# Kernel optimization log

Measured on AMD Instinct MI355X. Metric: run time of the kernel, lower is better.

## Reference

```python
import jax, jax.numpy as jnp
import numpy as np

EPS = 1e-5

def adder2d(x, w, stride=1, padding=1):
    # x: [B,C,H,W], w: [O,C,K,K]. AdderNet: out = -sum_{c,kh,kw} |x_patch - w|
    B, C, H, W = x.shape
    O, _, K, _ = w.shape
    xp = jnp.pad(x, ((0, 0), (0, 0), (padding, padding), (padding, padding)))
    Ho = (H + 2 * padding - K) // stride + 1
    Wo = (W + 2 * padding - K) // stride + 1
    out = jnp.zeros((B, O, Ho, Wo), x.dtype)
    for kh in range(K):  # fixed small loop over kernel taps (K*K = 9)
        for kw in range(K):
            xs = xp[:, :, kh:kh + stride * Ho:stride, kw:kw + stride * Wo:stride]  # [B,C,Ho,Wo]
            # broadcasted L1 distance over channel dim: [B,O,C,Ho,Wo] -> sum over C
            out = out - jnp.abs(xs[:, None, :, :, :] - w[None, :, :, kh, kw, None, None]).sum(axis=2)
    return out

def batchnorm(x, gamma, beta, mean, var):
    inv = gamma / jnp.sqrt(var + EPS)
    return x * inv[None, :, None, None] + (beta - mean * inv)[None, :, None, None]

def setup_inputs() -> dict:
    key = jax.random.key(0)
    ks = jax.random.split(key, 8)
    C = 64
    x = jax.random.normal(ks[0], (32, C, 32, 32), dtype=jnp.float32)
    w1 = jax.random.normal(ks[1], (C, C, 3, 3), dtype=jnp.float32) * 0.1
    w2 = jax.random.normal(ks[2], (C, C, 3, 3), dtype=jnp.float32) * 0.1
    bn1_gamma = jax.random.normal(ks[3], (C,), dtype=jnp.float32) * 0.1 + 1.0
    bn1_beta = jax.random.normal(ks[4], (C,), dtype=jnp.float32) * 0.1
    bn1_mean = jax.random.normal(ks[5], (C,), dtype=jnp.float32) * 0.1
    bn1_var = jax.random.uniform(ks[6], (C,), dtype=jnp.float32, minval=0.5, maxval=1.5)
    bn2_gamma = jnp.ones((C,), jnp.float32)
    bn2_beta = jnp.zeros((C,), jnp.float32)
    bn2_mean = jnp.zeros((C,), jnp.float32)
    bn2_var = jax.random.uniform(ks[7], (C,), dtype=jnp.float32, minval=0.5, maxval=1.5)
    return {"x": x, "w1": w1, "w2": w2,
            "bn1_gamma": bn1_gamma, "bn1_beta": bn1_beta, "bn1_mean": bn1_mean, "bn1_var": bn1_var,
            "bn2_gamma": bn2_gamma, "bn2_beta": bn2_beta, "bn2_mean": bn2_mean, "bn2_var": bn2_var}

def reference(x, w1, w2, bn1_gamma, bn1_beta, bn1_mean, bn1_var,
              bn2_gamma, bn2_beta, bn2_mean, bn2_var):
    out = adder2d(jax.nn.relu(batchnorm(x, bn1_gamma, bn1_beta, bn1_mean, bn1_var)), w1, stride=1, padding=1)
    # dropout_rate = 0.0 -> identity
    out = adder2d(jax.nn.relu(batchnorm(out, bn2_gamma, bn2_beta, bn2_mean, bn2_var)), w2, stride=1, padding=1)
    return out + x  # identity shortcut (stride=1, in_planes==planes)
```

## Files before the change

### kernel.cpp

```cpp
#include <hip/hip_runtime.h>
#include <stdint.h>

#define EPS 1e-5f

constexpr int B = 32, C = 64, O = 64, H = 32, W = 32;
constexpr int HP = 34, WP = 34;
constexpr int APLANE = HP * WP;
constexpr int CP = C / 2;
constexpr int AIMG2 = CP * APLANE;
constexpr int ASZ2  = B * AIMG2;
constexpr int WREP2 = (O / 4) * CP * 4 * 9;

constexpr float SCALE = 4096.0f;
constexpr float INV_SCALE = 1.0f / 4096.0f;
constexpr uint32_t ZP16 = 2048u;
constexpr uint32_t ZPAIR = ZP16 | (ZP16 << 16);

__device__ __forceinline__ uint32_t quant_act(float v) {
    return (uint32_t)(v * SCALE + 0.5f) + ZP16;
}
__device__ __forceinline__ uint32_t quant_w(float v) {
    return (uint32_t)(__float2int_rn(v * SCALE) + (int)ZP16);
}

#define SAD16(accv, av, wv) \
    asm("v_sad_u16 %0, %1, %2, %3" : "=v"(accv) : "v"(av), "s"(wv), "0"(accv))

__device__ __forceinline__ bool zero_prop(
    const float* g2, const float* be2, const float* m2, const float* v2)
{
    const int o = threadIdx.x & 63;
    const float inv  = g2[o] / sqrtf(v2[o] + EPS);
    const float bias = be2[o] - m2[o] * inv;
    const bool ok = (inv >= 0.f) && (bias < 0.5f / SCALE);
    return __ballot(ok) == ~0ull;
}

__global__ __launch_bounds__(256) void fused_kernel(
    const float* __restrict__ x,
    const float* __restrict__ w1, const float* __restrict__ w2,
    const float* __restrict__ g1, const float* __restrict__ be1,
    const float* __restrict__ m1, const float* __restrict__ v1,
    const float* __restrict__ g2, const float* __restrict__ be2,
    const float* __restrict__ m2, const float* __restrict__ v2,
    float* __restrict__ out,
    uint32_t* __restrict__ a2p,
    uint32_t* __restrict__ w1r, uint32_t* __restrict__ w2r,
    uint32_t* __restrict__ wsum2, uint32_t* __restrict__ flags,
    float* __restrict__ bn1c, float* __restrict__ bn2c)
{
    if (zero_prop(g2, be2, m2, v2)) {
        const int bo  = blockIdx.x;
        const int o   = bo & 63;
        const int t   = threadIdx.x;
        uint32_t s = 0;
        for (int k = t; k < C * 9; k += 256) {
            const uint32_t q = quant_w(w2[(size_t)o * C * 9 + k]);
            s += (q > ZP16) ? (q - ZP16) : (ZP16 - q);
        }
#pragma unroll
        for (int off = 32; off >= 1; off >>= 1) s += __shfl_down(s, off);
        __shared__ uint32_t red[4];
        if ((t & 63) == 0) red[t >> 6] = s;
        __syncthreads();
        const float wsv = (float)(red[0] + red[1] + red[2] + red[3]) * INV_SCALE;
        const size_t p = (size_t)bo * 256 + t;
        float4 v = ((const float4*)x)[p];
        v.x -= wsv; v.y -= wsv; v.z -= wsv; v.w -= wsv;
        ((float4*)out)[p] = v;
        return;
    }

    const int tid = blockIdx.x * 256 + threadIdx.x;
    const int nth = gridDim.x * 256;

    if (tid < O * 64) {
        const int o  = tid >> 6;
        const int ln = tid & 63;
        uint32_t s = 0;
        for (int k = ln; k < C * 9; k += 64) {
            const uint32_t q = quant_w(w2[(size_t)o * C * 9 + k]);
            s += (q > ZP16) ? (q - ZP16) : (ZP16 - q);
        }
        for (int off = 32; off >= 1; off >>= 1) s += __shfl_down(s, off);
        if (ln == 0) wsum2[o] = s;
    }

    for (int idx = tid; idx < WREP2; idx += nth) {
        const int k  = idx % 9;
        const int t2 = idx / 9;
        const int oi = t2 % 4;
        const int t3 = t2 / 4;
        const int cp = t3 % CP;
        const int og = t3 / CP;
        const int o  = og * 4 + oi;
        const uint32_t lo1 = quant_w(w1[((size_t)o * C + 2 * cp) * 9 + k]);
        const uint32_t hi1 = quant_w(w1[((size_t)o * C + 2 * cp + 1) * 9 + k]);
        const uint32_t lo2 = quant_w(w2[((size_t)o * C + 2 * cp) * 9 + k]);
        const uint32_t hi2 = quant_w(w2[((size_t)o * C + 2 * cp + 1) * 9 + k]);
        w1r[idx] = lo1 | (hi1 << 16);
        w2r[idx] = lo2 | (hi2 << 16);
    }
    if (tid < C) {
        const float i1 = g1[tid] / sqrtf(v1[tid] + EPS);
        bn1c[2 * tid]     = i1;
        bn1c[2 * tid + 1] = be1[tid] - m1[tid] * i1;
        const float i2 = g2[tid] / sqrtf(v2[tid] + EPS);
        bn2c[2 * tid]     = i2;
        bn2c[2 * tid + 1] = be2[tid] - m2[tid] * i2;
    }
    for (int idx = tid; idx < B * H; idx += nth) flags[idx] = 0;

    for (int idx = tid; idx < B * CP * 2 * WP; idx += nth) {
        const int col  = idx % WP;
        const int t2   = idx / WP;
        const int rsel = t2 % 2;
        const int bcp  = t2 / 2;
        a2p[(size_t)bcp * APLANE + (rsel ? HP - 1 : 0) * WP + col] = ZPAIR;
    }
    for (int idx = tid; idx < B * CP * 2 * H; idx += nth) {
        const int rr   = idx % H;
        const int t2   = idx / H;
        const int csel = t2 % 2;
        const int bcp  = t2 / 2;
        a2p[(size_t)bcp * APLANE + (rr + 1) * WP + (csel ? WP - 1 : 0)] = ZPAIR;
    }
}

__global__ __launch_bounds__(1024, 4) void adder1_kernel(
    const float* __restrict__ x, const uint32_t* __restrict__ wr,
    uint32_t* __restrict__ out, const float* __restrict__ bn1c,
    const float* __restrict__ bn2c, uint32_t* __restrict__ flags,
    const float* __restrict__ g2, const float* __restrict__ be2,
    const float* __restrict__ m2, const float* __restrict__ v2)
{
    if (zero_prop(g2, be2, m2, v2)) return;

    const int tid  = threadIdx.x;
    const int lane = tid & 63;
    const int w    = lane & 31;
    const int sub  = lane >> 5;
    const int og      = __builtin_amdgcn_readfirstlane(tid >> 6);
    const int rowbase = blockIdx.x * 4;
    const int b       = blockIdx.y;

    __shared__ uint32_t As[CP][6][WP];
    constexpr int LDSN = CP * 6 * WP;
    const float2* bc1 = (const float2*)bn1c;
#pragma unroll
    for (int i = 0; i < 7; ++i) {
        const int idx = tid + i * 1024;
        if (idx < LDSN) {
            const int col = idx % WP;
            const int seg = idx / WP;
            const int r   = seg % 6;
            const int cp  = seg / 6;
            const int prow = rowbase + r;
            uint32_t q0 = ZP16, q1 = ZP16;
            if (prow >= 1 && prow <= H && col >= 1 && col <= W) {
                const float* xb = x + (((size_t)b * C + 2 * cp) * H + (prow - 1)) * W
                                    + (col - 1);
                const float2 c0 = bc1[2 * cp];
                const float2 c1 = bc1[2 * cp + 1];
                q0 = quant_act(fmaxf(xb[0]     * c0.x + c0.y, 0.f));
                q1 = quant_act(fmaxf(xb[H * W] * c1.x + c1.y, 0.f));
            }
            As[cp][r][col] = q0 | (q1 << 16);
        }
    }
    __syncthreads();

    const uint32_t* wb = wr + (size_t)og * (CP * 36);
    uint32_t acc[4][2] = {};
#pragma unroll
    for (int cp = 0; cp < CP; ++cp) {
        uint32_t wg[36];
#pragma unroll
        for (int k = 0; k < 36; ++k) wg[k] = wb[cp * 36 + k];
#pragma unroll
        for (int kh = 0; kh < 3; ++kh)
#pragma unroll
        for (int kw = 0; kw < 3; ++kw)
#pragma unroll
        for (int oi = 0; oi < 4; ++oi)
#pragma unroll
        for (int r = 0; r < 2; ++r)
            SAD16(acc[oi][r], As[cp][sub * 2 + r + kh][w + kw],
                  wg[oi * 9 + kh * 3 + kw]);
    }

    const int row0 = rowbase + sub * 2;
    const float2* bc2 = (const float2*)bn2c;
    uint32_t qp[2][2];
#pragma unroll
    for (int p = 0; p < 2; ++p) {
        const int o0 = og * 4 + 2 * p;
        const float2 c0 = bc2[o0];
        const float2 c1 = bc2[o0 + 1];
#pragma unroll
        for (int r = 0; r < 2; ++r) {
            const float y0 = fmaxf(-(float)acc[2 * p][r]     * INV_SCALE * c0.x + c0.y, 0.f);
            const float y1 = fmaxf(-(float)acc[2 * p + 1][r] * INV_SCALE * c1.x + c1.y, 0.f);
            qp[p][r] = quant_act(y0) | (quant_act(y1) << 16);
        }
        uint32_t* op = out + (size_t)b * AIMG2 + (og * 2 + p) * APLANE
                           + (row0 + 1) * WP + (w + 1);
        op[0]  = qp[p][0];
        op[WP] = qp[p][1];
    }
    const unsigned long long b0 = __ballot((qp[0][0] | qp[1][0]) != ZPAIR);
    const unsigned long long b1 = __ballot((qp[0][1] | qp[1][1]) != ZPAIR);
    if (lane == 0) {
        uint32_t* fb = flags + (size_t)b * H + rowbase;
        if (b0 & 0xffffffffull) atomicOr(fb + 0, 1u);
        if (b1 & 0xffffffffull) atomicOr(fb + 1, 1u);
        if (b0 >> 32)           atomicOr(fb + 2, 1u);
        if (b1 >> 32)           atomicOr(fb + 3, 1u);
    }
}

__global__ __launch_bounds__(256, 4) void adder2_kernel(
    const uint32_t* __restrict__ ain, const uint32_t* __restrict__ wr,
    float* __restrict__ out, const float* __restrict__ xres,
    const uint32_t* __restrict__ flags, const uint32_t* __restrict__ wsum2,
    const float* __restrict__ g2, const float* __restrict__ be2,
    const float* __restrict__ m2, const float* __restrict__ v2)
{
    if (zero_prop(g2, be2, m2, v2)) return;

    const int tid  = threadIdx.x;
    const int b    = blockIdx.z;
    const int lane = tid & 63;
    const int wave = tid >> 6;
    const int w    = lane & 31;
    const int sub  = lane >> 5;
    const int og      = __builtin_amdgcn_readfirstlane(blockIdx.x * 4 + wave);
    const int rowbase = blockIdx.y * 4;
    const int row0    = rowbase + sub * 2;

    {
        uint32_t f = 0;
        const int rlo = (rowbase - 1 < 0) ? 0 : rowbase - 1;
        const int rhi = (rowbase + 4 > H - 1) ? H - 1 : rowbase + 4;
        for (int rr = rlo; rr <= rhi; ++rr) f |= flags[(size_t)b * H + rr];
        if (f == 0u) {
#pragma unroll
            for (int oi = 0; oi < 4; ++oi) {
                const int o = og * 4 + oi;
                const float wsv = (float)wsum2[o] * INV_SCALE;
                const float* xp = xres + (((size_t)b * C + o) * H + row0) * W + w;
                float* op = out + (((size_t)b * O + o) * H + row0) * W + w;
                op[0] = xp[0] - wsv;
                op[W] = xp[W] - wsv;
            }
            return;
        }
    }

    __shared__ uint32_t As[CP][6][WP];
    {
        const uint32_t* ab0 = ain + (size_t)b * AIMG2 + rowbase * WP;
#pragma unroll
        for (int i = 0; i < 26; ++i) {
            const int idx = tid + i * 256;
            if (idx < CP * 6 * WP) {
                const int col = idx % WP;
                const int seg = idx / WP;
                const int r   = seg % 6;
                const int cp  = seg / 6;
                As[cp][r][col] = ab0[(size_t)cp * APLANE + r * WP + col];
            }
        }
    }
    __syncthreads();

    const uint32_t* wb = wr + (size_t)og * (CP * 36);
    uint32_t acc[4][2] = {};
#pragma unroll
    for (int cp = 0; cp < CP; ++cp) {
        uint32_t wg[36];
#pragma unroll
        for (int k = 0; k < 36; ++k) wg[k] = wb[cp * 36 + k];
#pragma unroll
        for (int kh = 0; kh < 3; ++kh)
#pragma unroll
        for (int kw = 0; kw < 3; ++kw)
#pragma unroll
        for (int oi = 0; oi < 4; ++oi)
#pragma unroll
        for (int r = 0; r < 2; ++r)
            SAD16(acc[oi][r], As[cp][sub * 2 + r + kh][w + kw],
                  wg[oi * 9 + kh * 3 + kw]);
    }

#pragma unroll
    for (int oi = 0; oi < 4; ++oi) {
        const int o = og * 4 + oi;
        const float* xp = xres + (((size_t)b * C + o) * H + row0) * W + w;
        float* op = out + (((size_t)b * O + o) * H + row0) * W + w;
#pragma unroll
        for (int r = 0; r < 2; ++r)
            op[r * W] = xp[r * W] - (float)acc[oi][r] * INV_SCALE;
    }
}

extern "C" void kernel_launch(void* const* d_in, const int* in_sizes, int n_in,
                              void* d_out, int out_size, void* d_ws, size_t ws_size,
                              hipStream_t stream)
{
    const float* x   = (const float*)d_in[0];
    const float* w1  = (const float*)d_in[1];
    const float* w2  = (const float*)d_in[2];
    const float* g1  = (const float*)d_in[3];
    const float* be1 = (const float*)d_in[4];
    const float* m1  = (const float*)d_in[5];
    const float* v1  = (const float*)d_in[6];
    const float* g2  = (const float*)d_in[7];
    const float* be2 = (const float*)d_in[8];
    const float* m2  = (const float*)d_in[9];
    const float* v2  = (const float*)d_in[10];

    uint32_t* ws    = (uint32_t*)d_ws;
    uint32_t* a2p   = ws;
    uint32_t* w1r   = a2p + (size_t)ASZ2;
    uint32_t* w2r   = w1r + WREP2;
    uint32_t* wsum2 = w2r + WREP2;
    uint32_t* flags = wsum2 + O;
    float*    bn1c  = (float*)(flags + B * H);
    float*    bn2c  = bn1c + 2 * C;

    fused_kernel<<<B * O, 256, 0, stream>>>(x, w1, w2, g1, be1, m1, v1,
                                            g2, be2, m2, v2, (float*)d_out,
                                            a2p, w1r, w2r, wsum2, flags,
                                            bn1c, bn2c);
    adder1_kernel<<<dim3(8, 32), 1024, 0, stream>>>(x, w1r, a2p, bn1c, bn2c,
                                                    flags, g2, be2, m2, v2);
    adder2_kernel<<<dim3(4, 8, 32), 256, 0, stream>>>(a2p, w2r, (float*)d_out,
                                                      x, flags, wsum2,
                                                      g2, be2, m2, v2);
}
```

Measured before the change: 13.62 us.

## Merge three kernels into one persistent kernel with grid-wide barriers

Combines the setup, first adder and second adder kernels into a single 256-block, 1024-thread kernel. The stages are separated by atomic-counter grid barriers, and the barrier counter and flags are cleared with a memset. In the zero-propagation fast path, each block now computes eight weight sums itself and writes a 2048-float4 slice of x minus the weight sum. The aim is to remove the extra kernel launches and the near-empty early-exit kernels. The cost is a memset launch, spin-wait barriers that depend on all blocks being resident at once, and fewer, larger blocks.

```diff
diff --git a/kernel.cpp b/kernel.cpp
--- a/kernel.cpp
+++ b/kernel.cpp
@@ -10,6 +10,7 @@
 constexpr int AIMG2 = CP * APLANE;
 constexpr int ASZ2  = B * AIMG2;
 constexpr int WREP2 = (O / 4) * CP * 4 * 9;
+constexpr int NBLK  = 256;
 
 constexpr float SCALE = 4096.0f;
 constexpr float INV_SCALE = 1.0f / 4096.0f;
@@ -36,7 +37,19 @@
     return __ballot(ok) == ~0ull;
 }
 
-__global__ __launch_bounds__(256) void fused_kernel(
+__device__ __forceinline__ void grid_sync(uint32_t* bar) {
+    __syncthreads();
+    if (threadIdx.x == 0) {
+        __threadfence();
+        __hip_atomic_fetch_add(bar, 1u, __ATOMIC_RELEASE,
+                               __HIP_MEMORY_SCOPE_AGENT);
+        while (__hip_atomic_load(bar, __ATOMIC_ACQUIRE,
+                                 __HIP_MEMORY_SCOPE_AGENT) < (uint32_t)NBLK) {}
+    }
+    __syncthreads();
+}
+
+__global__ __launch_bounds__(1024, 4) void mono_kernel(
     const float* __restrict__ x,
     const float* __restrict__ w1, const float* __restrict__ w2,
     const float* __restrict__ g1, const float* __restrict__ be1,
@@ -44,49 +57,52 @@
     const float* __restrict__ g2, const float* __restrict__ be2,
     const float* __restrict__ m2, const float* __restrict__ v2,
     float* __restrict__ out,
+    uint32_t* __restrict__ bar, uint32_t* __restrict__ flags,
     uint32_t* __restrict__ a2p,
     uint32_t* __restrict__ w1r, uint32_t* __restrict__ w2r,
-    uint32_t* __restrict__ wsum2, uint32_t* __restrict__ flags,
+    uint32_t* __restrict__ wsum2,
     float* __restrict__ bn1c, float* __restrict__ bn2c)
 {
+    const int tid = threadIdx.x;
+    const int blk = blockIdx.x;
+
+    __shared__ uint32_t As[CP][6][WP];
+    __shared__ float wsv_s[8];
+
     if (zero_prop(g2, be2, m2, v2)) {
-        const int bo  = blockIdx.x;
-        const int o   = bo & 63;
-        const int t   = threadIdx.x;
-        uint32_t s = 0;
-        for (int k = t; k < C * 9; k += 256) {
-            const uint32_t q = quant_w(w2[(size_t)o * C * 9 + k]);
-            s += (q > ZP16) ? (q - ZP16) : (ZP16 - q);
-        }
-#pragma unroll
-        for (int off = 32; off >= 1; off >>= 1) s += __shfl_down(s, off);
-        __shared__ uint32_t red[4];
-        if ((t & 63) == 0) red[t >> 6] = s;
+        const int wv = tid >> 6, ln = tid & 63;
+        const int o0 = (blk & 7) * 8;
+        if (wv < 8) {
+            const int o = o0 + wv;
+            uint32_t s = 0;
+#pragma unroll
+            for (int k = ln; k < C * 9; k += 64) {
+                const uint32_t q = quant_w(w2[(size_t)o * (C * 9) + k]);
+                s += (q > ZP16) ? (q - ZP16) : (ZP16 - q);
+            }
+#pragma unroll
+            for (int off = 32; off >= 1; off >>= 1) s += __shfl_down(s, off);
+            if (ln == 0) wsv_s[wv] = (float)s * INV_SCALE;
+        }
         __syncthreads();
-        const float wsv = (float)(red[0] + red[1] + red[2] + red[3]) * INV_SCALE;
-        const size_t p = (size_t)bo * 256 + t;
-        float4 v = ((const float4*)x)[p];
-        v.x -= wsv; v.y -= wsv; v.z -= wsv; v.w -= wsv;
-        ((float4*)out)[p] = v;
+        const float4* xv = (const float4*)x;
+        float4* ov = (float4*)out;
+        const size_t base = (size_t)blk * 2048;
+#pragma unroll
+        for (int i = 0; i < 2; ++i) {
+            const int idx = tid + i * 1024;
+            const float wsv = wsv_s[idx >> 8];
+            float4 v = xv[base + idx];
+            v.x -= wsv; v.y -= wsv; v.z -= wsv; v.w -= wsv;
+            ov[base + idx] = v;
+        }
         return;
     }
 
-    const int tid = blockIdx.x * 256 + threadIdx.x;
-    const int nth = gridDim.x * 256;
-
-    if (tid < O * 64) {
-        const int o  = tid >> 6;
-        const int ln = tid & 63;
-        uint32_t s = 0;
-        for (int k = ln; k < C * 9; k += 64) {
-            const uint32_t q = quant_w(w2[(size_t)o * C * 9 + k]);
-            s += (q > ZP16) ? (q - ZP16) : (ZP16 - q);
-        }
-        for (int off = 32; off >= 1; off >>= 1) s += __shfl_down(s, off);
-        if (ln == 0) wsum2[o] = s;
-    }
-
-    for (int idx = tid; idx < WREP2; idx += nth) {
+    const int gtid = blk * 1024 + tid;
+    const int nth  = NBLK * 1024;
+
+    for (int idx = gtid; idx < WREP2; idx += nth) {
         const int k  = idx % 9;
         const int t2 = idx / 9;
         const int oi = t2 % 4;
@@ -101,143 +117,126 @@
         w1r[idx] = lo1 | (hi1 << 16);
         w2r[idx] = lo2 | (hi2 << 16);
     }
-    if (tid < C) {
-        const float i1 = g1[tid] / sqrtf(v1[tid] + EPS);
-        bn1c[2 * tid]     = i1;
-        bn1c[2 * tid + 1] = be1[tid] - m1[tid] * i1;
-        const float i2 = g2[tid] / sqrtf(v2[tid] + EPS);
-        bn2c[2 * tid]     = i2;
-        bn2c[2 * tid + 1] = be2[tid] - m2[tid] * i2;
-    }
-    for (int idx = tid; idx < B * H; idx += nth) flags[idx] = 0;
-
-    for (int idx = tid; idx < B * CP * 2 * WP; idx += nth) {
+    if (gtid < O * 64) {
+        const int o  = gtid >> 6;
+        const int ln = gtid & 63;
+        uint32_t s = 0;
+        for (int k = ln; k < C * 9; k += 64) {
+            const uint32_t q = quant_w(w2[(size_t)o * (C * 9) + k]);
+            s += (q > ZP16) ? (q - ZP16) : (ZP16 - q);
+        }
+        for (int off = 32; off >= 1; off >>= 1) s += __shfl_down(s, off);
+        if (ln == 0) wsum2[o] = s;
+    }
+    if (gtid < C) {
+        const float i1 = g1[gtid] / sqrtf(v1[gtid] + EPS);
+        bn1c[2 * gtid]     = i1;
+        bn1c[2 * gtid + 1] = be1[gtid] - m1[gtid] * i1;
+        const float i2 = g2[gtid] / sqrtf(v2[gtid] + EPS);
+        bn2c[2 * gtid]     = i2;
+        bn2c[2 * gtid + 1] = be2[gtid] - m2[gtid] * i2;
+    }
+    for (int idx = gtid; idx < B * CP * 2 * WP; idx += nth) {
         const int col  = idx % WP;
         const int t2   = idx / WP;
         const int rsel = t2 % 2;
         const int bcp  = t2 / 2;
         a2p[(size_t)bcp * APLANE + (rsel ? HP - 1 : 0) * WP + col] = ZPAIR;
     }
-    for (int idx = tid; idx < B * CP * 2 * H; idx += nth) {
+    for (int idx = gtid; idx < B * CP * 2 * H; idx += nth) {
         const int rr   = idx % H;
         const int t2   = idx / H;
         const int csel = t2 % 2;
         const int bcp  = t2 / 2;
         a2p[(size_t)bcp * APLANE + (rr + 1) * WP + (csel ? WP - 1 : 0)] = ZPAIR;
     }
-}
-
-__global__ __launch_bounds__(1024, 4) void adder1_kernel(
-    const float* __restrict__ x, const uint32_t* __restrict__ wr,
-    uint32_t* __restrict__ out, const float* __restrict__ bn1c,
-    const float* __restrict__ bn2c, uint32_t* __restrict__ flags,
-    const float* __restrict__ g2, const float* __restrict__ be2,
-    const float* __restrict__ m2, const float* __restrict__ v2)
-{
-    if (zero_prop(g2, be2, m2, v2)) return;
-
-    const int tid  = threadIdx.x;
+
+    grid_sync(bar + 0);
+
     const int lane = tid & 63;
     const int w    = lane & 31;
     const int sub  = lane >> 5;
     const int og      = __builtin_amdgcn_readfirstlane(tid >> 6);
-    const int rowbase = blockIdx.x * 4;
-    const int b       = blockIdx.y;
-
-    __shared__ uint32_t As[CP][6][WP];
+    const int rowbase = (blk & 7) * 4;
+    const int b       = blk >> 3;
     constexpr int LDSN = CP * 6 * WP;
-    const float2* bc1 = (const float2*)bn1c;
-#pragma unroll
-    for (int i = 0; i < 7; ++i) {
-        const int idx = tid + i * 1024;
-        if (idx < LDSN) {
-            const int col = idx % WP;
-            const int seg = idx / WP;
-            const int r   = seg % 6;
-            const int cp  = seg / 6;
-            const int prow = rowbase + r;
-            uint32_t q0 = ZP16, q1 = ZP16;
-            if (prow >= 1 && prow <= H && col >= 1 && col <= W) {
-                const float* xb = x + (((size_t)b * C + 2 * cp) * H + (prow - 1)) * W
-                                    + (col - 1);
-                const float2 c0 = bc1[2 * cp];
-                const float2 c1 = bc1[2 * cp + 1];
-                q0 = quant_act(fmaxf(xb[0]     * c0.x + c0.y, 0.f));
-                q1 = quant_act(fmaxf(xb[H * W] * c1.x + c1.y, 0.f));
-            }
-            As[cp][r][col] = q0 | (q1 << 16);
-        }
-    }
-    __syncthreads();
-
-    const uint32_t* wb = wr + (size_t)og * (CP * 36);
-    uint32_t acc[4][2] = {};
-#pragma unroll
-    for (int cp = 0; cp < CP; ++cp) {
-        uint32_t wg[36];
-#pragma unroll
-        for (int k = 0; k < 36; ++k) wg[k] = wb[cp * 36 + k];
-#pragma unroll
-        for (int kh = 0; kh < 3; ++kh)
-#pragma unroll
-        for (int kw = 0; kw < 3; ++kw)
-#pragma unroll
-        for (int oi = 0; oi < 4; ++oi)
-#pragma unroll
-        for (int r = 0; r < 2; ++r)
-            SAD16(acc[oi][r], As[cp][sub * 2 + r + kh][w + kw],
-                  wg[oi * 9 + kh * 3 + kw]);
-    }
+    {
+        const float2* bc1 = (const float2*)bn1c;
+#pragma unroll
+        for (int i = 0; i < 7; ++i) {
+            const int idx = tid + i * 1024;
+            if (idx < LDSN) {
+                const int col = idx % WP;
+                const int seg = idx / WP;
+                const int r   = seg % 6;
+                const int cp  = seg / 6;
+                const int prow = rowbase + r;
+                uint32_t q0 = ZP16, q1 = ZP16;
+                if (prow >= 1 && prow <= H && col >= 1 && col <= W) {
+                    const float* xb = x + (((size_t)b * C + 2 * cp) * H + (prow - 1)) * W
+                                        + (col - 1);
+                    const float2 c0 = bc1[2 * cp];
+                    const float2 c1 = bc1[2 * cp + 1];
+                    q0 = quant_act(fmaxf(xb[0]     * c0.x + c0.y, 0.f));
+                    q1 = quant_act(fmaxf(xb[H * W] * c1.x + c1.y, 0.f));
+                }
+                As[cp][r][col] = q0 | (q1 << 16);
+            }
+        }
+        __syncthreads();
+
+        const uint32_t* wb = w1r + (size_t)og * (CP * 36);
+        uint32_t acc[4][2] = {};
+#pragma unroll
+        for (int cp = 0; cp < CP; ++cp) {
+            uint32_t wg[36];
+#pragma unroll
+            for (int k = 0; k < 36; ++k) wg[k] = wb[cp * 36 + k];
+#pragma unroll
+            for (int kh = 0; kh < 3; ++kh)
+#pragma unroll
+            for (int kw = 0; kw < 3; ++kw)
+#pragma unroll
+            for (int oi = 0; oi < 4; ++oi)
+#pragma unroll
+            for (int r = 0; r < 2; ++r)
+                SAD16(acc[oi][r], As[cp][sub * 2 + r + kh][w + kw],
+                      wg[oi * 9 + kh * 3 + kw]);
+        }
+
+        const int row0 = rowbase + sub * 2;
+        const float2* bc2 = (const float2*)bn2c;
+        uint32_t qp[2][2];
+#pragma unroll
+        for (int p = 0; p < 2; ++p) {
+            const int o0 = og * 4 + 2 * p;
+            const float2 c0 = bc2[o0];
+            const float2 c1 = bc2[o0 + 1];
+#pragma unroll
+            for (int r = 0; r < 2; ++r) {
+                const float y0 = fmaxf(-(float)acc[2 * p][r]     * INV_SCALE * c0.x + c0.y, 0.f);
+                const float y1 = fmaxf(-(float)acc[2 * p + 1][r] * INV_SCALE * c1.x + c1.y, 0.f);
+                qp[p][r] = quant_act(y0) | (quant_act(y1) << 16);
+            }
+            uint32_t* op = a2p + (size_t)b * AIMG2 + (og * 2 + p) * APLANE
+                               + (row0 + 1) * WP + (w + 1);
+            op[0]  = qp[p][0];
+            op[WP] = qp[p][1];
+        }
+        const unsigned long long b0 = __ballot((qp[0][0] | qp[1][0]) != ZPAIR);
+        const unsigned long long b1 = __ballot((qp[0][1] | qp[1][1]) != ZPAIR);
+        if (lane == 0) {
+            uint32_t* fb = flags + (size_t)b * H + rowbase;
+            if (b0 & 0xffffffffull) atomicOr(fb + 0, 1u);
+            if (b1 & 0xffffffffull) atomicOr(fb + 1, 1u);
+            if (b0 >> 32)           atomicOr(fb + 2, 1u);
+            if (b1 >> 32)           atomicOr(fb + 3, 1u);
+        }
+    }
+
+    grid_sync(bar + 1);
 
     const int row0 = rowbase + sub * 2;
-    const float2* bc2 = (const float2*)bn2c;
-    uint32_t qp[2][2];
-#pragma unroll
-    for (int p = 0; p < 2; ++p) {
-        const int o0 = og * 4 + 2 * p;
-        const float2 c0 = bc2[o0];
-        const float2 c1 = bc2[o0 + 1];
-#pragma unroll
-        for (int r = 0; r < 2; ++r) {
-            const float y0 = fmaxf(-(float)acc[2 * p][r]     * INV_SCALE * c0.x + c0.y, 0.f);
-            const float y1 = fmaxf(-(float)acc[2 * p + 1][r] * INV_SCALE * c1.x + c1.y, 0.f);
-            qp[p][r] = quant_act(y0) | (quant_act(y1) << 16);
-        }
-        uint32_t* op = out + (size_t)b * AIMG2 + (og * 2 + p) * APLANE
-                           + (row0 + 1) * WP + (w + 1);
-        op[0]  = qp[p][0];
-        op[WP] = qp[p][1];
-    }
-    const unsigned long long b0 = __ballot((qp[0][0] | qp[1][0]) != ZPAIR);
-    const unsigned long long b1 = __ballot((qp[0][1] | qp[1][1]) != ZPAIR);
-    if (lane == 0) {
-        uint32_t* fb = flags + (size_t)b * H + rowbase;
-        if (b0 & 0xffffffffull) atomicOr(fb + 0, 1u);
-        if (b1 & 0xffffffffull) atomicOr(fb + 1, 1u);
-        if (b0 >> 32)           atomicOr(fb + 2, 1u);
-        if (b1 >> 32)           atomicOr(fb + 3, 1u);
-    }
-}
-
-__global__ __launch_bounds__(256, 4) void adder2_kernel(
-    const uint32_t* __restrict__ ain, const uint32_t* __restrict__ wr,
-    float* __restrict__ out, const float* __restrict__ xres,
-    const uint32_t* __restrict__ flags, const uint32_t* __restrict__ wsum2,
-    const float* __restrict__ g2, const float* __restrict__ be2,
-    const float* __restrict__ m2, const float* __restrict__ v2)
-{
-    if (zero_prop(g2, be2, m2, v2)) return;
-
-    const int tid  = threadIdx.x;
-    const int b    = blockIdx.z;
-    const int lane = tid & 63;
-    const int wave = tid >> 6;
-    const int w    = lane & 31;
-    const int sub  = lane >> 5;
-    const int og      = __builtin_amdgcn_readfirstlane(blockIdx.x * 4 + wave);
-    const int rowbase = blockIdx.y * 4;
-    const int row0    = rowbase + sub * 2;
-
     {
         uint32_t f = 0;
         const int rlo = (rowbase - 1 < 0) ? 0 : rowbase - 1;
@@ -248,7 +247,7 @@
             for (int oi = 0; oi < 4; ++oi) {
                 const int o = og * 4 + oi;
                 const float wsv = (float)wsum2[o] * INV_SCALE;
-                const float* xp = xres + (((size_t)b * C + o) * H + row0) * W + w;
+                const float* xp = x + (((size_t)b * C + o) * H + row0) * W + w;
                 float* op = out + (((size_t)b * O + o) * H + row0) * W + w;
                 op[0] = xp[0] - wsv;
                 op[W] = xp[W] - wsv;
@@ -256,14 +255,12 @@
             return;
         }
     }
-
-    __shared__ uint32_t As[CP][6][WP];
     {
-        const uint32_t* ab0 = ain + (size_t)b * AIMG2 + rowbase * WP;
-#pragma unroll
-        for (int i = 0; i < 26; ++i) {
-            const int idx = tid + i * 256;
-            if (idx < CP * 6 * WP) {
+        const uint32_t* ab0 = a2p + (size_t)b * AIMG2 + rowbase * WP;
+#pragma unroll
+        for (int i = 0; i < 7; ++i) {
+            const int idx = tid + i * 1024;
+            if (idx < LDSN) {
                 const int col = idx % WP;
                 const int seg = idx / WP;
                 const int r   = seg % 6;
@@ -274,7 +271,7 @@
     }
     __syncthreads();
 
-    const uint32_t* wb = wr + (size_t)og * (CP * 36);
+    const uint32_t* wb = w2r + (size_t)og * (CP * 36);
     uint32_t acc[4][2] = {};
 #pragma unroll
     for (int cp = 0; cp < CP; ++cp) {
@@ -296,7 +293,7 @@
 #pragma unroll
     for (int oi = 0; oi < 4; ++oi) {
         const int o = og * 4 + oi;
-        const float* xp = xres + (((size_t)b * C + o) * H + row0) * W + w;
+        const float* xp = x + (((size_t)b * C + o) * H + row0) * W + w;
         float* op = out + (((size_t)b * O + o) * H + row0) * W + w;
 #pragma unroll
         for (int r = 0; r < 2; ++r)
@@ -321,21 +318,19 @@
     const float* v2  = (const float*)d_in[10];
 
     uint32_t* ws    = (uint32_t*)d_ws;
-    uint32_t* a2p   = ws;
+    uint32_t* bar   = ws;
+    uint32_t* flags = ws + 2;
+    uint32_t* a2p   = flags + B * H;
     uint32_t* w1r   = a2p + (size_t)ASZ2;
     uint32_t* w2r   = w1r + WREP2;
     uint32_t* wsum2 = w2r + WREP2;
-    uint32_t* flags = wsum2 + O;
-    float*    bn1c  = (float*)(flags + B * H);
+    float*    bn1c  = (float*)(wsum2 + O);
     float*    bn2c  = bn1c + 2 * C;
 
-    fused_kernel<<<B * O, 256, 0, stream>>>(x, w1, w2, g1, be1, m1, v1,
-                                            g2, be2, m2, v2, (float*)d_out,
-                                            a2p, w1r, w2r, wsum2, flags,
-                                            bn1c, bn2c);
-    adder1_kernel<<<dim3(8, 32), 1024, 0, stream>>>(x, w1r, a2p, bn1c, bn2c,
-                                                    flags, g2, be2, m2, v2);
-    adder2_kernel<<<dim3(4, 8, 32), 256, 0, stream>>>(a2p, w2r, (float*)d_out,
-                                                      x, flags, wsum2,
-                                                      g2, be2, m2, v2);
-}
+    hipMemsetAsync(bar, 0, (2 + B * H) * sizeof(uint32_t), stream);
+
+    mono_kernel<<<NBLK, 1024, 0, stream>>>(x, w1, w2, g1, be1, m1, v1,
+                                           g2, be2, m2, v2, (float*)d_out,
+                                           bar, flags, a2p, w1r, w2r, wsum2,
+                                           bn1c, bn2c);
+}
```

Result: slower. 16.16 us (+18.6%).
